# Kernel tuning notes

Hardware: AMD Instinct MI355X
Metric: run time of the kernel (lower is better)

Reference implementation:

```python
import jax, jax.numpy as jnp
import numpy as np

# static config (matches init_kwargs)
PL, LAT, LON = 8, 48, 96
WP, WL, WW = 2, 6, 12
SP, SL, SN = 1, 3, 6
NH = 16


def _earth_position_index(ws):
    wp, wl, ww = ws
    zi = np.arange(wp); zj = -np.arange(wp) * wp
    hi = np.arange(wl); hj = -np.arange(wl) * wl
    w = np.arange(ww)
    c1 = np.stack(np.meshgrid(zi, hi, w, indexing='ij')).reshape(3, -1)
    c2 = np.stack(np.meshgrid(zj, hj, w, indexing='ij')).reshape(3, -1)
    coords = (c1[:, :, None] - c2[:, None, :]).transpose(1, 2, 0).astype(np.int64)
    coords[:, :, 2] += ww - 1
    coords[:, :, 1] *= 2 * ww - 1
    coords[:, :, 0] *= (2 * ww - 1) * wl * wl
    return coords.sum(-1)  # (N, N)

_POS_IDX = jnp.asarray(_earth_position_index((WP, WL, WW)))


def _ln(x, w, b, eps=1e-5):
    m = x.mean(-1, keepdims=True)
    v = x.var(-1, keepdims=True)
    return (x - m) / jnp.sqrt(v + eps) * w + b


def setup_inputs() -> dict:
    key = jax.random.key(0)
    ks = jax.random.split(key, 8)
    B, C = 1, 512
    L = PL * LAT * LON
    TOW = (PL // WP) * (LAT // WL)
    TBL = WP * WP * WL * WL * (2 * WW - 1)
    s = 0.02
    return {
        'x': jax.random.normal(ks[0], (B, L, C), jnp.float32),
        'norm1_w': jnp.ones((C,), jnp.float32), 'norm1_b': jnp.zeros((C,), jnp.float32),
        'qkv_w': jax.random.normal(ks[1], (C, 3 * C), jnp.float32) * s,
        'qkv_b': jnp.zeros((3 * C,), jnp.float32),
        'proj_w': jax.random.normal(ks[2], (C, C), jnp.float32) * s,
        'proj_b': jnp.zeros((C,), jnp.float32),
        'bias_table': jax.random.normal(ks[3], (TBL, TOW, NH), jnp.float32) * s,
        'norm2_w': jnp.ones((C,), jnp.float32), 'norm2_b': jnp.zeros((C,), jnp.float32),
        'mlp_w1': jax.random.normal(ks[4], (C, 4 * C), jnp.float32) * s,
        'mlp_b1': jnp.zeros((4 * C,), jnp.float32),
        'mlp_w2': jax.random.normal(ks[5], (4 * C, C), jnp.float32) * s,
        'mlp_b2': jnp.zeros((C,), jnp.float32),
    }


def reference(x, norm1_w, norm1_b, qkv_w, qkv_b, proj_w, proj_b, bias_table,
              norm2_w, norm2_b, mlp_w1, mlp_b1, mlp_w2, mlp_b2):
    B, L, C = x.shape
    HD = C // NH
    scale = HD ** -0.5
    N = WP * WL * WW
    nPl, nLat, nLon = PL // WP, LAT // WL, LON // WW
    nW = nPl * nLat

    # norm1 + roll + window partition (B, nLon, nPl, nLat, wp, wl, ww, C)
    h = _ln(x, norm1_w, norm1_b).reshape(B, PL, LAT, LON, C)
    h = jnp.roll(h, (-SP, -SL, -SN), axis=(1, 2, 3))
    h = h.reshape(B, nPl, WP, nLat, WL, nLon, WW, C)
    h = h.transpose(0, 5, 1, 3, 2, 4, 6, 7).reshape(B * nLon, nW, N, C)

    # attention
    qkv = (h @ qkv_w + qkv_b).reshape(B * nLon, nW, N, 3, NH, HD)
    qkv = qkv.transpose(3, 0, 4, 1, 2, 5)  # (3, B_, nh, nW, N, hd)
    q, k, v = qkv[0] * scale, qkv[1], qkv[2]
    attn = jnp.einsum('bhwnd,bhwmd->bhwnm', q, k)
    bias = bias_table[_POS_IDX.reshape(-1)].reshape(N, N, nW, NH)
    bias = bias.transpose(3, 2, 0, 1)  # (nh, nW, N, N)
    attn = jax.nn.softmax(attn + bias[None], axis=-1)
    o = jnp.einsum('bhwnm,bhwmd->bhwnd', attn, v)
    o = o.transpose(0, 2, 3, 1, 4).reshape(B * nLon, nW, N, C)
    o = o @ proj_w + proj_b

    # reverse partition + roll back
    o = o.reshape(B, nLon, nPl, nLat, WP, WL, WW, C)
    o = o.transpose(0, 2, 4, 3, 5, 1, 6, 7).reshape(B, PL, LAT, LON, C)
    o = jnp.roll(o, (SP, SL, SN), axis=(1, 2, 3)).reshape(B, L, C)

    x = x + o
    h2 = _ln(x, norm2_w, norm2_b)
    h2 = jax.nn.gelu(h2 @ mlp_w1 + mlp_b1, approximate=False) @ mlp_w2 + mlp_b2
    return x + h2
```

## Files before the change

kernel.cpp:

```cpp
#include <hip/hip_runtime.h>
#include <hip/hip_bf16.h>
#include <math.h>

typedef __bf16 bf16;
typedef __attribute__((ext_vector_type(8))) __bf16 bf16x8;
typedef __attribute__((ext_vector_type(4))) float f32x4;
typedef __attribute__((ext_vector_type(8))) float f32x8;

#define NTOK   36864
#define CDIM   512
#define NHEAD  16
#define HD     32
#define NWIN   32
#define NLON   8
#define WTOK   144
#define TBL    3312

#define GLOAD_LDS16(g, l) __builtin_amdgcn_global_load_lds( \
    (const __attribute__((address_space(1))) void*)(const void*)(g), \
    (__attribute__((address_space(3))) void*)(l), 16, 0, 0)

#define SWZ(o) ((o) ^ ((((o) >> 7) & 3) << 4))

__device__ __forceinline__ int src_token(int r) {
    int ww_ = r % 12; int q = r / 12;
    int wl_ = q % 6;  q /= 6;
    int wp_ = q & 1;  q >>= 1;
    int lat_g = q & 7; q >>= 3;
    int pl_g = q & 3;  q >>= 2;
    int lon_g = q;
    int pl  = pl_g * 2 + wp_ + 1;  if (pl  >= 8)  pl  -= 8;
    int lat = lat_g * 6 + wl_ + 3; if (lat >= 48) lat -= 48;
    int lon = lon_g * 12 + ww_ + 6; if (lon >= 96) lon -= 96;
    return (pl * 48 + lat) * 96 + lon;
}

__device__ __forceinline__ float gelu_exact(float x) {
    return 0.5f * x * (1.0f + erff(x * 0.70710678118654752f));
}

__global__ __launch_bounds__(256) void transpose_f32_bf16(const float* __restrict__ in,
                                                          bf16* __restrict__ out,
                                                          int R, int Cc) {
    __shared__ bf16 tile[32][33];
    int c0 = blockIdx.x * 32, r0 = blockIdx.y * 32;
    int tx = threadIdx.x & 31, ty = threadIdx.x >> 5;
#pragma unroll
    for (int i = 0; i < 32; i += 8)
        tile[ty + i][tx] = (bf16)in[(size_t)(r0 + ty + i) * Cc + c0 + tx];
    __syncthreads();
#pragma unroll
    for (int i = 0; i < 32; i += 8)
        out[(size_t)(c0 + ty + i) * R + r0 + tx] = tile[tx][ty + i];
}

__global__ __launch_bounds__(256) void table_transpose(const float* __restrict__ in,
                                                       float* __restrict__ outT) {
    __shared__ float tile[32][33];
    int i0 = blockIdx.x * 32, w0 = blockIdx.y * 32;
    int tx = threadIdx.x & 31, ty = threadIdx.x >> 5;
#pragma unroll
    for (int r = 0; r < 32; r += 8)
        if (i0 + ty + r < TBL) tile[ty + r][tx] = in[(size_t)(i0 + ty + r) * 512 + w0 + tx];
    __syncthreads();
#pragma unroll
    for (int r = 0; r < 32; r += 8)
        if (i0 + tx < TBL) outT[(size_t)(w0 + ty + r) * TBL + i0 + tx] = tile[tx][ty + r];
}

template<bool PERM>
__global__ __launch_bounds__(256) void ln_kernel(const float* __restrict__ in,
                                                 const float* __restrict__ w,
                                                 const float* __restrict__ b,
                                                 bf16* __restrict__ out) {
    int r = blockIdx.x * 4 + (threadIdx.x >> 6);
    int lane = threadIdx.x & 63;
    int s = PERM ? src_token(r) : r;
    f32x8 v8 = *(const f32x8*)(in + (size_t)s * CDIM + lane * 8);
    float sum = 0.f, sq = 0.f;
#pragma unroll
    for (int i = 0; i < 8; ++i) { sum += v8[i]; sq += v8[i] * v8[i]; }
#pragma unroll
    for (int m = 1; m < 64; m <<= 1) { sum += __shfl_xor(sum, m); sq += __shfl_xor(sq, m); }
    float mean = sum * (1.f / 512.f);
    float var  = sq  * (1.f / 512.f) - mean * mean;
    float rstd = rsqrtf(var + 1e-5f);
    f32x8 w8 = *(const f32x8*)(w + lane * 8);
    f32x8 b8 = *(const f32x8*)(b + lane * 8);
    bf16x8 o8;
#pragma unroll
    for (int i = 0; i < 8; ++i)
        o8[i] = (bf16)((v8[i] - mean) * rstd * w8[i] + b8[i]);
    *(bf16x8*)(out + (size_t)r * CDIM + lane * 8) = o8;
}

template<int EPI>
__global__ __launch_bounds__(256) void gemm_bt(const bf16* __restrict__ A,
                                               const bf16* __restrict__ Bt,
                                               const float* __restrict__ bias,
                                               void* __restrict__ Cout_,
                                               const float* __restrict__ X,
                                               int K, int N, int gx) {
    __shared__ bf16 As[3 * 4096];
    __shared__ bf16 Bs[3 * 4096];
    int t = threadIdx.x;
    int wid = t >> 6, lane = t & 63;
    int wr = wid >> 1, wc = wid & 1;
    int g = lane >> 4, cl = lane & 15;

    int nwg = gridDim.x, orig = blockIdx.x;
    int wg = orig;
    if ((nwg & 7) == 0) {
        int cpx = nwg >> 3;
        wg = (orig & 7) * cpx + (orig >> 3);
    }
    int m0 = (wg / gx) * 128, n0 = (wg % gx) * 128;
    f32x4 acc[4][4] = {};

    int el = lane ^ ((lane >> 3) & 3);
    int srow = wid * 16 + (el >> 2);
    int scol = (el & 3) * 8;
    const bf16* Ag0 = A  + (size_t)(m0 + srow) * K + scol;
    const bf16* Ag1 = Ag0 + (size_t)64 * K;
    const bf16* Bg0 = Bt + (size_t)(n0 + srow) * K + scol;
    const bf16* Bg1 = Bg0 + (size_t)64 * K;
    int ldsoff = wid * 512;

#define STAGE_TILE(kt, buf) do {                       \
        int kk = (kt) << 5;                            \
        bf16* Ad = As + (buf) * 4096;                  \
        bf16* Bd = Bs + (buf) * 4096;                  \
        GLOAD_LDS16(Ag0 + kk, Ad + ldsoff);            \
        GLOAD_LDS16(Ag1 + kk, Ad + 2048 + ldsoff);     \
        GLOAD_LDS16(Bg0 + kk, Bd + ldsoff);            \
        GLOAD_LDS16(Bg1 + kk, Bd + 2048 + ldsoff);     \
    } while (0)

    int nt = K >> 5;
    STAGE_TILE(0, 0);
    STAGE_TILE(1, 1);
    asm volatile("s_waitcnt vmcnt(4) lgkmcnt(0)" ::: "memory");
    __builtin_amdgcn_s_barrier();

    const char* Ab = (const char*)As;
    const char* Bb = (const char*)Bs;
    int cur = 0;
    for (int kt = 0; kt < nt; ++kt) {
        if (kt + 2 < nt) STAGE_TILE(kt + 2, (kt + 2) % 3);
        int cbase = cur * 8192;
        bf16x8 af[4], bfv[4];
#pragma unroll
        for (int i = 0; i < 4; ++i) {
            int off = cbase + (wr * 64 + i * 16 + cl) * 64 + g * 16;
            af[i]  = *(const bf16x8*)(Ab + SWZ(off));
        }
#pragma unroll
        for (int i = 0; i < 4; ++i) {
            int off = cbase + (wc * 64 + i * 16 + cl) * 64 + g * 16;
            bfv[i] = *(const bf16x8*)(Bb + SWZ(off));
        }
#pragma unroll
        for (int mi = 0; mi < 4; ++mi)
#pragma unroll
            for (int ni = 0; ni < 4; ++ni)
                acc[mi][ni] = __builtin_amdgcn_mfma_f32_16x16x32_bf16(af[mi], bfv[ni], acc[mi][ni], 0, 0, 0);
        asm volatile("s_waitcnt vmcnt(4) lgkmcnt(0)" ::: "memory");
        __builtin_amdgcn_s_barrier();
        cur = (cur == 2) ? 0 : cur + 1;
    }
#undef STAGE_TILE

#pragma unroll
    for (int mi = 0; mi < 4; ++mi) {
#pragma unroll
        for (int j = 0; j < 4; ++j) {
            int row = m0 + wr * 64 + mi * 16 + g * 4 + j;
            int srw = 0;
            if (EPI == 2) srw = src_token(row);
#pragma unroll
            for (int ni = 0; ni < 4; ++ni) {
                int col = n0 + wc * 64 + ni * 16 + cl;
                float v = acc[mi][ni][j] + bias[col];
                if (EPI == 1) v = gelu_exact(v);
                if (EPI == 0 || EPI == 1) {
                    ((bf16*)Cout_)[(size_t)row * N + col] = (bf16)v;
                } else if (EPI == 2) {
                    size_t o = (size_t)srw * CDIM + col;
                    ((float*)Cout_)[o] = X[o] + v;
                } else {
                    size_t o = (size_t)row * N + col;
                    ((float*)Cout_)[o] += v;
                }
            }
        }
    }
}

__global__ __launch_bounds__(256) void attn_mfma(const bf16* __restrict__ qkv,
                                                 const float* __restrict__ tableT,
                                                 bf16* __restrict__ obuf) {
    int h = blockIdx.x, w = blockIdx.y, b_ = blockIdx.z;
    int t = threadIdx.x, wid = t >> 6, lane = t & 63;
    int g = lane >> 4, cl = lane & 15;
    size_t base = ((size_t)b_ * NWIN + w) * WTOK;

    __shared__ bf16 P[WTOK * 168];
    __shared__ bf16 vT[32 * 168];
    __shared__ float bias_s[TBL];
    bf16* qs = P;
    bf16* ks = P + WTOK * 40;

    const bf16* qg = qkv + base * 1536 + h * 32;
    for (int tok = t >> 2; tok < WTOK; tok += 64) {
        int c8 = (t & 3) * 8;
        *(bf16x8*)(qs + tok * 40 + c8) = *(const bf16x8*)(qg + (size_t)tok * 1536 + c8);
        *(bf16x8*)(ks + tok * 40 + c8) = *(const bf16x8*)(qg + 512 + (size_t)tok * 1536 + c8);
        bf16x8 v8 = *(const bf16x8*)(qg + 1024 + (size_t)tok * 1536 + c8);
#pragma unroll
        for (int i = 0; i < 8; ++i) vT[(c8 + i) * 168 + tok] = v8[i];
    }
    for (int z = t; z < 32 * 24; z += 256) vT[(z / 24) * 168 + 144 + (z % 24)] = (bf16)0.f;
    const float* tb = tableT + (size_t)(w * 16 + h) * TBL;
    for (int i = t; i < TBL; i += 256) bias_s[i] = tb[i];
    __syncthreads();

    f32x4 sacc[3][9] = {};
    bf16x8 kf[9];
#pragma unroll
    for (int ct = 0; ct < 9; ++ct)
        kf[ct] = *(const bf16x8*)(ks + (ct * 16 + cl) * 40 + g * 8);
#pragma unroll
    for (int rti = 0; rti < 3; ++rti) {
        int rt = wid + rti * 4;
        if (rt < 9) {
            bf16x8 qf = *(const bf16x8*)(qs + (rt * 16 + cl) * 40 + g * 8);
#pragma unroll
            for (int ct = 0; ct < 9; ++ct)
                sacc[rti][ct] = __builtin_amdgcn_mfma_f32_16x16x32_bf16(qf, kf[ct], sacc[rti][ct], 0, 0, 0);
        }
    }
    __syncthreads();

    for (int z = t; z < WTOK * 24; z += 256) P[(z / 24) * 168 + 144 + (z % 24)] = (bf16)0.f;

    int bm[9];
#pragma unroll
    for (int ct = 0; ct < 9; ++ct) {
        int m = ct * 16 + cl;
        int wm = m % 12, tm = m / 12, hm = tm % 6, zm = tm / 6;
        bm[ct] = zm * 1656 + hm * 138 + 11 - wm;
    }

    const float scale = 0.17677669529663689f;
    float rinv[3][4];
#pragma unroll
    for (int rti = 0; rti < 3; ++rti) {
        int rt = wid + rti * 4;
        if (rt < 9) {
#pragma unroll
            for (int j = 0; j < 4; ++j) {
                int row = rt * 16 + g * 4 + j;
                int wn = row % 12, tn = row / 12, hn = tn % 6, zn = tn / 6;
                int an = zn * 828 + hn * 23 + wn;
                float mx = -1e30f;
#pragma unroll
                for (int ct = 0; ct < 9; ++ct) {
                    float v = sacc[rti][ct][j] * scale + bias_s[an + bm[ct]];
                    sacc[rti][ct][j] = v;
                    mx = fmaxf(mx, v);
                }
                for (int msk = 1; msk < 16; msk <<= 1) mx = fmaxf(mx, __shfl_xor(mx, msk));
                float sm = 0.f;
#pragma unroll
                for (int ct = 0; ct < 9; ++ct) {
                    float p = __expf(sacc[rti][ct][j] - mx);
                    sm += p;
                    P[row * 168 + ct * 16 + cl] = (bf16)p;
                }
                for (int msk = 1; msk < 16; msk <<= 1) sm += __shfl_xor(sm, msk);
                rinv[rti][j] = 1.f / sm;
            }
        }
    }
    __syncthreads();

#pragma unroll
    for (int rti = 0; rti < 3; ++rti) {
        int rt = wid + rti * 4;
        if (rt < 9) {
            f32x4 oacc[2] = {};
#pragma unroll
            for (int ks_ = 0; ks_ < 5; ++ks_) {
                bf16x8 pf = *(const bf16x8*)(P + (rt * 16 + cl) * 168 + ks_ * 32 + g * 8);
#pragma unroll
                for (int c2 = 0; c2 < 2; ++c2) {
                    bf16x8 vf = *(const bf16x8*)(vT + (c2 * 16 + cl) * 168 + ks_ * 32 + g * 8);
                    oacc[c2] = __builtin_amdgcn_mfma_f32_16x16x32_bf16(pf, vf, oacc[c2], 0, 0, 0);
                }
            }
#pragma unroll
            for (int c2 = 0; c2 < 2; ++c2)
#pragma unroll
                for (int j = 0; j < 4; ++j) {
                    int row = rt * 16 + g * 4 + j;
                    obuf[(base + row) * CDIM + h * 32 + c2 * 16 + cl] =
                        (bf16)(oacc[c2][j] * rinv[rti][j]);
                }
        }
    }
}

extern "C" void kernel_launch(void* const* d_in, const int* in_sizes, int n_in,
                              void* d_out, int out_size, void* d_ws, size_t ws_size,
                              hipStream_t stream) {
    const float* x       = (const float*)d_in[0];
    const float* n1w     = (const float*)d_in[1];
    const float* n1b     = (const float*)d_in[2];
    const float* qkv_w   = (const float*)d_in[3];
    const float* qkv_b   = (const float*)d_in[4];
    const float* proj_w  = (const float*)d_in[5];
    const float* proj_b  = (const float*)d_in[6];
    const float* btab    = (const float*)d_in[7];
    const float* n2w     = (const float*)d_in[8];
    const float* n2b     = (const float*)d_in[9];
    const float* mlp_w1  = (const float*)d_in[10];
    const float* mlp_b1  = (const float*)d_in[11];
    const float* mlp_w2  = (const float*)d_in[12];
    const float* mlp_b2  = (const float*)d_in[13];
    float* out = (float*)d_out;

    const size_t OFF_HBUF = 0;
    const size_t OFF_QKV  = 37748736;
    const size_t OFF_TT   = 150994944;
    const size_t OFF_OBUF = 188743680;
    const size_t OFF_WTQ  = 226492416;
    const size_t OFF_WTP  = 228065280;
    const size_t OFF_WT1  = 228589568;
    const size_t OFF_WT2  = 230686720;
    const size_t NEED     = 232783872;

    if (ws_size < NEED) return;

    char* ws = (char*)d_ws;
    bf16*  hbuf   = (bf16*)(ws + OFF_HBUF);
    bf16*  qkvbuf = (bf16*)(ws + OFF_QKV);
    bf16*  midbuf = qkvbuf;
    float* tableT = (float*)(ws + OFF_TT);
    bf16*  obuf   = (bf16*)(ws + OFF_OBUF);
    bf16*  wtq    = (bf16*)(ws + OFF_WTQ);
    bf16*  wtp    = (bf16*)(ws + OFF_WTP);
    bf16*  wt1    = (bf16*)(ws + OFF_WT1);
    bf16*  wt2    = (bf16*)(ws + OFF_WT2);

    transpose_f32_bf16<<<dim3(1536 / 32, 512 / 32), 256, 0, stream>>>(qkv_w, wtq, 512, 1536);
    transpose_f32_bf16<<<dim3(512 / 32, 512 / 32), 256, 0, stream>>>(proj_w, wtp, 512, 512);
    transpose_f32_bf16<<<dim3(2048 / 32, 512 / 32), 256, 0, stream>>>(mlp_w1, wt1, 512, 2048);
    transpose_f32_bf16<<<dim3(512 / 32, 2048 / 32), 256, 0, stream>>>(mlp_w2, wt2, 2048, 512);
    table_transpose<<<dim3((TBL + 31) / 32, 512 / 32), 256, 0, stream>>>(btab, tableT);

    ln_kernel<true><<<NTOK / 4, 256, 0, stream>>>(x, n1w, n1b, hbuf);

    gemm_bt<0><<<12 * 288, 256, 0, stream>>>(hbuf, wtq, qkv_b, qkvbuf, nullptr, 512, 1536, 12);

    attn_mfma<<<dim3(NHEAD, NWIN, NLON), 256, 0, stream>>>(qkvbuf, tableT, obuf);

    gemm_bt<2><<<4 * 288, 256, 0, stream>>>(obuf, wtp, proj_b, out, x, 512, 512, 4);

    ln_kernel<false><<<NTOK / 4, 256, 0, stream>>>(out, n2w, n2b, hbuf);

    gemm_bt<1><<<16 * 288, 256, 0, stream>>>(hbuf, wt1, mlp_b1, midbuf, nullptr, 512, 2048, 16);

    gemm_bt<3><<<4 * 288, 256, 0, stream>>>(midbuf, wt2, mlp_b2, out, nullptr, 2048, 512, 4);
}
```

Before: 582.2 us.

## Enlarge GEMM tile to 128x256 with 1x4 wave layout and wider LDS staging

Changes the bf16 GEMM workgroup tile from 128x128 to 128x256. Each of the four waves now covers all 128 rows and a 64-column strip, holding 8x4 accumulators, and the triple-buffered LDS stage grows to 24 KB per buffer. The goal is more MFMA work per LDS fragment load and per global byte, with half as many workgroups in every GEMM launch. In exchange it doubles accumulator registers, needs 72 KB of LDS per block (launch bounds ask for 2 blocks per CU), and leaves fewer blocks for the smaller GEMMs (576 for proj and MLP2).

```diff
diff --git a/kernel.cpp b/kernel.cpp
--- a/kernel.cpp
+++ b/kernel.cpp
@@ -95,18 +95,16 @@
 }
 
 template<int EPI>
-__global__ __launch_bounds__(256) void gemm_bt(const bf16* __restrict__ A,
-                                               const bf16* __restrict__ Bt,
-                                               const float* __restrict__ bias,
-                                               void* __restrict__ Cout_,
-                                               const float* __restrict__ X,
-                                               int K, int N, int gx) {
-    __shared__ bf16 As[3 * 4096];
-    __shared__ bf16 Bs[3 * 4096];
-    int t = threadIdx.x;
-    int wid = t >> 6, lane = t & 63;
-    int wr = wid >> 1, wc = wid & 1;
-    int g = lane >> 4, cl = lane & 15;
+__global__ __launch_bounds__(256, 2) void gemm_bt(const bf16* __restrict__ A,
+                                                  const bf16* __restrict__ Bt,
+                                                  const float* __restrict__ bias,
+                                                  void* __restrict__ Cout_,
+                                                  const float* __restrict__ X,
+                                                  int K, int N, int gx) {
+    __shared__ char lds[3 * 24576];
+    const int t = threadIdx.x;
+    const int wid = t >> 6, lane = t & 63;
+    const int g = lane >> 4, cl = lane & 15;
 
     int nwg = gridDim.x, orig = blockIdx.x;
     int wg = orig;
@@ -114,8 +112,9 @@
         int cpx = nwg >> 3;
         wg = (orig & 7) * cpx + (orig >> 3);
     }
-    int m0 = (wg / gx) * 128, n0 = (wg % gx) * 128;
-    f32x4 acc[4][4] = {};
+    const int m0 = (wg / gx) * 128, n0 = (wg % gx) * 256;
+
+    f32x4 acc[8][4] = {};
 
     int el = lane ^ ((lane >> 3) & 3);
     int srow = wid * 16 + (el >> 2);
@@ -124,63 +123,66 @@
     const bf16* Ag1 = Ag0 + (size_t)64 * K;
     const bf16* Bg0 = Bt + (size_t)(n0 + srow) * K + scol;
     const bf16* Bg1 = Bg0 + (size_t)64 * K;
-    int ldsoff = wid * 512;
-
-#define STAGE_TILE(kt, buf) do {                       \
-        int kk = (kt) << 5;                            \
-        bf16* Ad = As + (buf) * 4096;                  \
-        bf16* Bd = Bs + (buf) * 4096;                  \
-        GLOAD_LDS16(Ag0 + kk, Ad + ldsoff);            \
-        GLOAD_LDS16(Ag1 + kk, Ad + 2048 + ldsoff);     \
-        GLOAD_LDS16(Bg0 + kk, Bd + ldsoff);            \
-        GLOAD_LDS16(Bg1 + kk, Bd + 2048 + ldsoff);     \
+    const bf16* Bg2 = Bg0 + (size_t)128 * K;
+    const bf16* Bg3 = Bg0 + (size_t)192 * K;
+    const int wb = wid << 10;
+
+#define STAGE_TILE(kt, buf) do {                         \
+        int kk = (kt) << 5;                              \
+        char* bb = lds + (buf) * 24576;                  \
+        GLOAD_LDS16(Ag0 + kk, bb + wb);                  \
+        GLOAD_LDS16(Ag1 + kk, bb + 4096  + wb);          \
+        GLOAD_LDS16(Bg0 + kk, bb + 8192  + wb);          \
+        GLOAD_LDS16(Bg1 + kk, bb + 12288 + wb);          \
+        GLOAD_LDS16(Bg2 + kk, bb + 16384 + wb);          \
+        GLOAD_LDS16(Bg3 + kk, bb + 20480 + wb);          \
     } while (0)
 
-    int nt = K >> 5;
+    const int nt = K >> 5;
     STAGE_TILE(0, 0);
     STAGE_TILE(1, 1);
-    asm volatile("s_waitcnt vmcnt(4) lgkmcnt(0)" ::: "memory");
+    asm volatile("s_waitcnt vmcnt(6)" ::: "memory");
     __builtin_amdgcn_s_barrier();
 
-    const char* Ab = (const char*)As;
-    const char* Bb = (const char*)Bs;
     int cur = 0;
     for (int kt = 0; kt < nt; ++kt) {
         if (kt + 2 < nt) STAGE_TILE(kt + 2, (kt + 2) % 3);
-        int cbase = cur * 8192;
-        bf16x8 af[4], bfv[4];
-#pragma unroll
-        for (int i = 0; i < 4; ++i) {
-            int off = cbase + (wr * 64 + i * 16 + cl) * 64 + g * 16;
-            af[i]  = *(const bf16x8*)(Ab + SWZ(off));
-        }
-#pragma unroll
-        for (int i = 0; i < 4; ++i) {
-            int off = cbase + (wc * 64 + i * 16 + cl) * 64 + g * 16;
-            bfv[i] = *(const bf16x8*)(Bb + SWZ(off));
-        }
-#pragma unroll
-        for (int mi = 0; mi < 4; ++mi)
-#pragma unroll
-            for (int ni = 0; ni < 4; ++ni)
-                acc[mi][ni] = __builtin_amdgcn_mfma_f32_16x16x32_bf16(af[mi], bfv[ni], acc[mi][ni], 0, 0, 0);
-        asm volatile("s_waitcnt vmcnt(4) lgkmcnt(0)" ::: "memory");
+        const char* bb = lds + cur * 24576;
+        bf16x8 aF[8], bF[4];
+#pragma unroll
+        for (int i = 0; i < 8; ++i) {
+            int off = ((i * 16 + cl) << 6) + (g << 4);
+            aF[i] = *(const bf16x8*)(bb + SWZ(off));
+        }
+#pragma unroll
+        for (int fc = 0; fc < 4; ++fc) {
+            int grow = wid * 64 + fc * 16 + cl;
+            int off = ((grow & 127) << 6) + (g << 4);
+            bF[fc] = *(const bf16x8*)(bb + 8192 + ((grow >> 7) << 13) + SWZ(off));
+        }
+#pragma unroll
+        for (int i = 0; i < 8; ++i)
+#pragma unroll
+            for (int fc = 0; fc < 4; ++fc)
+                acc[i][fc] = __builtin_amdgcn_mfma_f32_16x16x32_bf16(aF[i], bF[fc], acc[i][fc], 0, 0, 0);
+        if (kt + 2 < nt) asm volatile("s_waitcnt vmcnt(6) lgkmcnt(0)" ::: "memory");
+        else             asm volatile("s_waitcnt vmcnt(0) lgkmcnt(0)" ::: "memory");
         __builtin_amdgcn_s_barrier();
         cur = (cur == 2) ? 0 : cur + 1;
     }
 #undef STAGE_TILE
 
 #pragma unroll
-    for (int mi = 0; mi < 4; ++mi) {
-#pragma unroll
-        for (int j = 0; j < 4; ++j) {
-            int row = m0 + wr * 64 + mi * 16 + g * 4 + j;
+    for (int i = 0; i < 8; ++i) {
+#pragma unroll
+        for (int jj = 0; jj < 4; ++jj) {
+            int row = m0 + i * 16 + g * 4 + jj;
             int srw = 0;
             if (EPI == 2) srw = src_token(row);
 #pragma unroll
-            for (int ni = 0; ni < 4; ++ni) {
-                int col = n0 + wc * 64 + ni * 16 + cl;
-                float v = acc[mi][ni][j] + bias[col];
+            for (int fc = 0; fc < 4; ++fc) {
+                int col = n0 + wid * 64 + fc * 16 + cl;
+                float v = acc[i][fc][jj] + bias[col];
                 if (EPI == 1) v = gelu_exact(v);
                 if (EPI == 0 || EPI == 1) {
                     ((bf16*)Cout_)[(size_t)row * N + col] = (bf16)v;
@@ -360,15 +362,15 @@
 
     ln_kernel<true><<<NTOK / 4, 256, 0, stream>>>(x, n1w, n1b, hbuf);
 
-    gemm_bt<0><<<12 * 288, 256, 0, stream>>>(hbuf, wtq, qkv_b, qkvbuf, nullptr, 512, 1536, 12);
+    gemm_bt<0><<<6 * 288, 256, 0, stream>>>(hbuf, wtq, qkv_b, qkvbuf, nullptr, 512, 1536, 6);
 
     attn_mfma<<<dim3(NHEAD, NWIN, NLON), 256, 0, stream>>>(qkvbuf, tableT, obuf);
 
-    gemm_bt<2><<<4 * 288, 256, 0, stream>>>(obuf, wtp, proj_b, out, x, 512, 512, 4);
+    gemm_bt<2><<<2 * 288, 256, 0, stream>>>(obuf, wtp, proj_b, out, x, 512, 512, 2);
 
     ln_kernel<false><<<NTOK / 4, 256, 0, stream>>>(out, n2w, n2b, hbuf);
 
-    gemm_bt<1><<<16 * 288, 256, 0, stream>>>(hbuf, wt1, mlp_b1, midbuf, nullptr, 512, 2048, 16);
-
-    gemm_bt<3><<<4 * 288, 256, 0, stream>>>(midbuf, wt2, mlp_b2, out, nullptr, 2048, 512, 4);
-}
+    gemm_bt<1><<<8 * 288, 256, 0, stream>>>(hbuf, wt1, mlp_b1, midbuf, nullptr, 512, 2048, 8);
+
+    gemm_bt<3><<<2 * 288, 256, 0, stream>>>(midbuf, wt2, mlp_b2, out, nullptr, 2048, 512, 2);
+}
```

Result: no change. 587.2 us (+0.9%).
